# Performance work log

Hardware: AMD Instinct MI355X
Metric: run time of the kernel (lower is better)

## Reference

```python
import jax, jax.numpy as jnp
import numpy as np

ITERS = 2
EPS = 1e-6

_OFFSETS = [(a, b, c) for a in (-1, 0, 1) for b in (-1, 0, 1) for c in (-1, 0, 1)]


def _erosion_step(im):
    # product over full 3x3x3 neighborhood (connectivity=26 -> all 27 voxels),
    # out-of-bounds padded with 1 (identity for product)
    B, C, D, H, W = im.shape
    p = jnp.pad(im, ((0, 0), (0, 0), (1, 1), (1, 1), (1, 1)), constant_values=1.0)
    prod = jnp.ones_like(im)
    for dz, dy, dx in _OFFSETS:
        prod = prod * p[:, :, 1 + dz:1 + dz + D, 1 + dy:1 + dy + H, 1 + dx:1 + dx + W]
    return prod


def _distance_map(im, iters=ITERS):
    # PositiveDistanceMap: dils = -SoftErosion3D(1-im) where SoftErosion3D
    # returns temp = -sum_k im_k (im_0 = 1-im, im_{k+1} = im_k * erosion(im_k))
    cur = 1.0 - im
    acc = jnp.zeros_like(cur)
    for _ in range(iters):
        acc = acc + cur
        cur = cur * _erosion_step(cur)
    return acc


def _lah_loss(x, y_onehot):
    axes = (2, 3, 4)  # batch_lah=False -> per (batch, class) reduction
    dm_hat = _distance_map(x)
    dm_gt = _distance_map(y_onehot)
    fp = (dm_gt * x).sum(axes)
    fn = (dm_hat * y_onehot).sum(axes)
    # norm == 0
    fp = fp / (x.sum(axes) + EPS)
    fn = fn / (y_onehot.sum(axes) + EPS)
    lah = (fp + fn + jnp.abs(fp - fn)) / 2  # logsum2 == elementwise max
    return lah[:, 1:].mean()  # do_bg=False drops background channel


def setup_inputs() -> dict:
    key = jax.random.key(0)
    k1, k2 = jax.random.split(key)
    x = jax.random.uniform(k1, (2, 4, 128, 128, 128), dtype=jnp.float32)
    y = jax.random.randint(k2, (2, 1, 128, 128, 128), 0, 4, dtype=jnp.int64)
    return {"x": x, "y": y}


def reference(x, y):
    C = x.shape[1]
    y_onehot = jax.nn.one_hot(y[:, 0], C, axis=1, dtype=x.dtype)  # [B,C,D,H,W]
    return _lah_loss(x, y_onehot)
```

## Files before the change

kernel.cpp:

```cpp
#include <hip/hip_runtime.h>

constexpr int SPB = 1 << 21;
constexpr float EPSV = 1e-6f;

__device__ unsigned char g_mask[2 * SPB];

constexpr int K0_ZSEG = 4;
constexpr int K0_NBLK = (2 * (128 / K0_ZSEG) * 128) / 4;

struct MEnt { int pk, cx, cy; };

__device__ __forceinline__ MEnt k0_load(const int* __restrict__ yb, int s,
                                        int rbase0, bool ym1, bool yp1) {
    MEnt e;
    const int rb = (s << 14) | rbase0;
    int2 vc = *(const int2*)(yb + rb);
    int nib0 = 1 << vc.x, nib1 = 1 << vc.y;
    if (ym1) { int2 vm = *(const int2*)(yb + rb - 128); nib0 |= 1 << vm.x; nib1 |= 1 << vm.y; }
    if (yp1) { int2 vp = *(const int2*)(yb + rb + 128); nib0 |= 1 << vp.x; nib1 |= 1 << vp.y; }
    e.pk = nib0 | (nib1 << 8);
    e.cx = vc.x; e.cy = vc.y;
    return e;
}

__global__ __launch_bounds__(256) void mask_build(const int* __restrict__ y32) {
    const int wid = (blockIdx.x << 2) | (threadIdx.x >> 6);
    const int lane = threadIdx.x & 63;
    const int yy = wid & 127;
    const int zs = (wid >> 7) & 31;
    const int b = (wid >> 12) & 1;
    const int x0 = lane << 1;
    const int z0 = zs * K0_ZSEG;
    const bool ym1 = yy > 0, yp1 = yy < 127;
    const int rbase0 = (yy << 7) | x0;

    const int* __restrict__ yb = y32 + ((long)b << 21);
    unsigned char* __restrict__ mb = g_mask + ((long)b << 21);

    MEnt e0, e1;
    if (z0 > 0) e0 = k0_load(yb, z0 - 1, rbase0, ym1, yp1);
    else { e0.pk = 0; e0.cx = 0; e0.cy = 0; }
    e1 = k0_load(yb, z0, rbase0, ym1, yp1);

#pragma unroll
    for (int dz = 0; dz < K0_ZSEG; ++dz) {
        const int z = z0 + dz;
        MEnt e2;
        if (z + 1 < 128) e2 = k0_load(yb, z + 1, rbase0, ym1, yp1);
        else { e2.pk = 0; e2.cx = 0; e2.cy = 0; }

        const int zor = e0.pk | e1.pk | e2.pk;
        int orL = __shfl_up(zor, 1);
        if (lane == 0) orL = 0;
        int orR = __shfl_down(zor, 1);
        if (lane == 63) orR = 0;
        const int full0 = (zor | (zor >> 8) | (orL >> 8)) & 15;
        const int full1 = (zor | (zor >> 8) | orR) & 15;

        const unsigned short st =
            (unsigned short)((full0 | (e1.cx << 4)) | ((full1 | (e1.cy << 4)) << 8));
        *(unsigned short*)(mb + ((z << 14) | rbase0)) = st;

        e0 = e1; e1 = e2;
    }
}

constexpr int NBLK = 1024;

__global__ __launch_bounds__(256) void lah_main(const float* __restrict__ x,
                                                float* __restrict__ acc) {
    __shared__ float raw[3][10][128];
    __shared__ float yp[3][8][128];
    __shared__ float sred[4];

    const int bid = blockIdx.x;
    const int plane = bid & 7;
    const int b = plane >> 2, cls = plane & 3;
    const int inner = bid >> 3;
    const int yc = inner & 15;
    const int zq = inner >> 4;
    const int r0 = yc * 8;
    const int z0 = zq * 16;
    const int t = threadIdx.x;
    const int rr = t >> 5;
    const int xc = (t & 31) << 2;
    const int lane = t & 63;

    const float* __restrict__ xp = x + ((long)plane << 21);
    const unsigned char* __restrict__ mb = g_mask + ((long)b << 21);
    const int mrow = (r0 + rr) << 7;

    auto slot = [](int k) -> int { return (k + 129) % 3; };

    auto gload = [&](int k, int i, int c4) -> float4 {
        const int gr = r0 - 1 + i;
        if ((unsigned)k > 127u || (unsigned)gr > 127u)
            return make_float4(0.f, 0.f, 0.f, 0.f);
        return *(const float4*)(xp + ((k << 14) | (gr << 7) | c4));
    };

    auto stage_direct = [&](int k) {
        const int s = slot(k);
        float4 v = gload(k, rr, xc);
        *(float4*)&raw[s][rr][xc] = v;
        if (t < 64) {
            const int i = 8 + (t >> 5);
            float4 w = gload(k, i, xc);
            *(float4*)&raw[s][i][xc] = w;
        }
    };

    auto do_yprod = [&](int k) {
        const int s = slot(k);
        const float4 a = *(const float4*)&raw[s][rr][xc];
        const float4 bq = *(const float4*)&raw[s][rr + 1][xc];
        const float4 c = *(const float4*)&raw[s][rr + 2][xc];
        float4 o;
        o.x = (1.f - a.x) * (1.f - bq.x) * (1.f - c.x);
        o.y = (1.f - a.y) * (1.f - bq.y) * (1.f - c.y);
        o.z = (1.f - a.z) * (1.f - bq.z) * (1.f - c.z);
        o.w = (1.f - a.w) * (1.f - bq.w) * (1.f - c.w);
        *(float4*)&yp[s][rr][xc] = o;
    };

    stage_direct(z0 - 1);
    stage_direct(z0);
    stage_direct(z0 + 1);
    __syncthreads();
    do_yprod(z0 - 1);
    do_yprod(z0);
    unsigned mcur = *(const unsigned*)(mb + ((z0 << 14) | mrow | xc));

    float fp = 0.f, fn = 0.f, sx = 0.f, sy = 0.f;

    for (int dz = 0; dz < 16; ++dz) {
        const int z = z0 + dz;

        float4 gA = gload(z + 2, rr, xc);
        float4 gB = make_float4(0.f, 0.f, 0.f, 0.f);
        if (t < 64) gB = gload(z + 2, 8 + (t >> 5), xc);
        unsigned mnext = 0;
        if (dz < 15)
            mnext = *(const unsigned*)(mb + (((z + 1) << 14) | mrow | xc));

        do_yprod(z + 1);
        __syncthreads();

        {
            const int sA = slot(z - 1), sB = slot(z), sC = slot(z + 1);
            const float4 a = *(const float4*)&yp[sA][rr][xc];
            const float4 bq = *(const float4*)&yp[sB][rr][xc];
            const float4 c = *(const float4*)&yp[sC][rr][xc];
            const float zp0 = a.x * bq.x * c.x;
            const float zp1 = a.y * bq.y * c.y;
            const float zp2 = a.z * bq.z * c.z;
            const float zp3 = a.w * bq.w * c.w;
            float zl = __shfl_up(zp3, 1);
            if ((t & 31) == 0) zl = 1.f;
            float zr = __shfl_down(zp0, 1);
            if ((t & 31) == 31) zr = 1.f;
            const float t01 = zp0 * zp1, t12 = zp1 * zp2, t23 = zp2 * zp3;
            const float P[4] = {zl * t01, t01 * zp2, t12 * zp3, t23 * zr};

            const float4 xv4 = *(const float4*)&raw[sB][rr + 1][xc];
            const float xa[4] = {xv4.x, xv4.y, xv4.z, xv4.w};
#pragma unroll
            for (int j = 0; j < 4; ++j) {
                const int m = (mcur >> (j * 8)) & 0xFF;
                const bool pres = (m >> cls) & 1;
                const bool eq = (m >> 4) == cls;
                const float xv = xa[j];
                sx += xv;
                fp += eq ? 0.f : xv * (pres ? 1.f : 2.f);
                fn += eq ? (1.f - xv) * (1.f + P[j]) : 0.f;
                sy += eq ? 1.f : 0.f;
            }
        }

        {
            const int s = slot(z + 2);
            *(float4*)&raw[s][rr][xc] = gA;
            if (t < 64) *(float4*)&raw[s][8 + (t >> 5)][xc] = gB;
        }
        __syncthreads();
        mcur = mnext;
    }

    float rr4[4] = {fp, fn, sx, sy};
#pragma unroll
    for (int i = 0; i < 4; ++i) {
        float vv = rr4[i];
#pragma unroll
        for (int off = 32; off >= 1; off >>= 1) vv += __shfl_down(vv, off);
        rr4[i] = vv;
    }
    if (t < 4) sred[t] = 0.f;
    __syncthreads();
    if (lane == 0) {
#pragma unroll
        for (int i = 0; i < 4; ++i) atomicAdd(&sred[i], rr4[i]);
    }
    __syncthreads();
    if (t < 4)
        atomicAdd(&acc[b * 16 + t * 4 + cls], sred[t]);
}

__global__ void lah_finalize(const float* __restrict__ acc, float* __restrict__ out) {
    float loss = 0.f;
#pragma unroll
    for (int b = 0; b < 2; ++b) {
#pragma unroll
        for (int c = 1; c < 4; ++c) {
            const float fp = acc[b * 16 + 0 + c];
            const float fn = acc[b * 16 + 4 + c];
            const float sxv = acc[b * 16 + 8 + c];
            const float syv = acc[b * 16 + 12 + c];
            loss += fmaxf(fp / (sxv + EPSV), fn / (syv + EPSV));
        }
    }
    out[0] = loss / 6.f;
}

extern "C" void kernel_launch(void* const* d_in, const int* in_sizes, int n_in,
                              void* d_out, int out_size, void* d_ws, size_t ws_size,
                              hipStream_t stream) {
    const float* x = (const float*)d_in[0];
    const int* y32 = (const int*)d_in[1];
    float* out = (float*)d_out;
    float* acc = (float*)d_ws;

    hipMemsetAsync(d_ws, 0, 32 * sizeof(float), stream);
    mask_build<<<K0_NBLK, 256, 0, stream>>>(y32);
    lah_main<<<NBLK, 256, 0, stream>>>(x, acc);
    lah_finalize<<<1, 1, 0, stream>>>(acc, out);
}
```

Before: 41.73 us.

## Keep y-products in registers, cut barriers per slice, shrink z-chunk

The shared-memory y-product buffer is dropped. Each thread already consumes only its own y-product values across consecutive z-slices, so they are now carried in registers and rotated along with the centre x values. The slice loop now needs one barrier per iteration instead of two, uses explicit rotating slot indices instead of a modulo, and is fully unrolled. The z-chunk per block is halved to 8, which doubles the block count for more parallelism at the cost of more z-halo reloads.

```diff
diff --git a/kernel.cpp b/kernel.cpp
--- a/kernel.cpp
+++ b/kernel.cpp
@@ -65,12 +65,12 @@
     }
 }
 
-constexpr int NBLK = 1024;
+constexpr int ZC = 8;
+constexpr int NBLK = 8 * 16 * (128 / ZC);
 
 __global__ __launch_bounds__(256) void lah_main(const float* __restrict__ x,
                                                 float* __restrict__ acc) {
     __shared__ float raw[3][10][128];
-    __shared__ float yp[3][8][128];
     __shared__ float sred[4];
 
     const int bid = blockIdx.x;
@@ -80,7 +80,7 @@
     const int yc = inner & 15;
     const int zq = inner >> 4;
     const int r0 = yc * 8;
-    const int z0 = zq * 16;
+    const int z0 = zq * ZC;
     const int t = threadIdx.x;
     const int rr = t >> 5;
     const int xc = (t & 31) << 2;
@@ -90,80 +90,71 @@
     const unsigned char* __restrict__ mb = g_mask + ((long)b << 21);
     const int mrow = (r0 + rr) << 7;
 
-    auto slot = [](int k) -> int { return (k + 129) % 3; };
-
-    auto gload = [&](int k, int i, int c4) -> float4 {
+    auto gload = [&](int k, int i) -> float4 {
         const int gr = r0 - 1 + i;
         if ((unsigned)k > 127u || (unsigned)gr > 127u)
             return make_float4(0.f, 0.f, 0.f, 0.f);
-        return *(const float4*)(xp + ((k << 14) | (gr << 7) | c4));
+        return *(const float4*)(xp + ((k << 14) | (gr << 7) | xc));
     };
-
-    auto stage_direct = [&](int k) {
-        const int s = slot(k);
-        float4 v = gload(k, rr, xc);
-        *(float4*)&raw[s][rr][xc] = v;
-        if (t < 64) {
-            const int i = 8 + (t >> 5);
-            float4 w = gload(k, i, xc);
-            *(float4*)&raw[s][i][xc] = w;
-        }
+    auto stage_direct = [&](int k, int s) {
+        *(float4*)&raw[s][rr][xc] = gload(k, rr);
+        if (t < 64) *(float4*)&raw[s][8 + (t >> 5)][xc] = gload(k, 8 + (t >> 5));
     };
-
-    auto do_yprod = [&](int k) {
-        const int s = slot(k);
+    auto yprod = [&](int s, float4& cx) -> float4 {
         const float4 a = *(const float4*)&raw[s][rr][xc];
         const float4 bq = *(const float4*)&raw[s][rr + 1][xc];
         const float4 c = *(const float4*)&raw[s][rr + 2][xc];
+        cx = bq;
         float4 o;
         o.x = (1.f - a.x) * (1.f - bq.x) * (1.f - c.x);
         o.y = (1.f - a.y) * (1.f - bq.y) * (1.f - c.y);
         o.z = (1.f - a.z) * (1.f - bq.z) * (1.f - c.z);
         o.w = (1.f - a.w) * (1.f - bq.w) * (1.f - c.w);
-        *(float4*)&yp[s][rr][xc] = o;
+        return o;
     };
 
-    stage_direct(z0 - 1);
-    stage_direct(z0);
-    stage_direct(z0 + 1);
+    stage_direct(z0 - 1, 0);
+    stage_direct(z0, 1);
+    stage_direct(z0 + 1, 2);
     __syncthreads();
-    do_yprod(z0 - 1);
-    do_yprod(z0);
+    float4 cxd, cx0;
+    float4 ypm1 = yprod(0, cxd);
+    float4 yp0 = yprod(1, cx0);
     unsigned mcur = *(const unsigned*)(mb + ((z0 << 14) | mrow | xc));
 
+    int sm = 0, s0 = 1, sp = 2;
+
     float fp = 0.f, fn = 0.f, sx = 0.f, sy = 0.f;
 
-    for (int dz = 0; dz < 16; ++dz) {
+#pragma unroll
+    for (int dz = 0; dz < ZC; ++dz) {
         const int z = z0 + dz;
-
-        float4 gA = gload(z + 2, rr, xc);
+        __syncthreads();
+
+        float4 gA = make_float4(0.f, 0.f, 0.f, 0.f);
         float4 gB = make_float4(0.f, 0.f, 0.f, 0.f);
-        if (t < 64) gB = gload(z + 2, 8 + (t >> 5), xc);
         unsigned mnext = 0;
-        if (dz < 15)
+        if (dz < ZC - 1) {
+            gA = gload(z + 2, rr);
+            if (t < 64) gB = gload(z + 2, 8 + (t >> 5));
             mnext = *(const unsigned*)(mb + (((z + 1) << 14) | mrow | xc));
-
-        do_yprod(z + 1);
-        __syncthreads();
+        }
+
+        float4 cx1;
+        const float4 ypp1 = yprod(sp, cx1);
 
         {
-            const int sA = slot(z - 1), sB = slot(z), sC = slot(z + 1);
-            const float4 a = *(const float4*)&yp[sA][rr][xc];
-            const float4 bq = *(const float4*)&yp[sB][rr][xc];
-            const float4 c = *(const float4*)&yp[sC][rr][xc];
-            const float zp0 = a.x * bq.x * c.x;
-            const float zp1 = a.y * bq.y * c.y;
-            const float zp2 = a.z * bq.z * c.z;
-            const float zp3 = a.w * bq.w * c.w;
+            const float zp0 = ypm1.x * yp0.x * ypp1.x;
+            const float zp1 = ypm1.y * yp0.y * ypp1.y;
+            const float zp2 = ypm1.z * yp0.z * ypp1.z;
+            const float zp3 = ypm1.w * yp0.w * ypp1.w;
             float zl = __shfl_up(zp3, 1);
             if ((t & 31) == 0) zl = 1.f;
             float zr = __shfl_down(zp0, 1);
             if ((t & 31) == 31) zr = 1.f;
             const float t01 = zp0 * zp1, t12 = zp1 * zp2, t23 = zp2 * zp3;
             const float P[4] = {zl * t01, t01 * zp2, t12 * zp3, t23 * zr};
-
-            const float4 xv4 = *(const float4*)&raw[sB][rr + 1][xc];
-            const float xa[4] = {xv4.x, xv4.y, xv4.z, xv4.w};
+            const float xa[4] = {cx0.x, cx0.y, cx0.z, cx0.w};
 #pragma unroll
             for (int j = 0; j < 4; ++j) {
                 const int m = (mcur >> (j * 8)) & 0xFF;
@@ -177,13 +168,13 @@
             }
         }
 
-        {
-            const int s = slot(z + 2);
-            *(float4*)&raw[s][rr][xc] = gA;
-            if (t < 64) *(float4*)&raw[s][8 + (t >> 5)][xc] = gB;
-        }
-        __syncthreads();
-        mcur = mnext;
+        if (dz < ZC - 1) {
+            *(float4*)&raw[sm][rr][xc] = gA;
+            if (t < 64) *(float4*)&raw[sm][8 + (t >> 5)][xc] = gB;
+        }
+
+        const int tmp = sm; sm = s0; s0 = sp; sp = tmp;
+        ypm1 = yp0; yp0 = ypp1; cx0 = cx1; mcur = mnext;
     }
 
     float rr4[4] = {fp, fn, sx, sy};
```

Result: slower. 50.60 us (+21.3%).
